# Performance work log

Measured on AMD Instinct MI355X. Metric: run time of the kernel, lower is better.

## Reference

```python
import jax, jax.numpy as jnp
import numpy as np

B, T, D_IN, H = 128, 256, 512, 1024

def setup_inputs() -> dict:
    key = jax.random.key(0)
    ks = jax.random.split(key, 12)
    s = 1.0 / np.sqrt(H)
    return {
        "input": jax.random.normal(ks[0], (B, T, D_IN), jnp.float32),
        "h0": jax.random.normal(ks[1], (B, H), jnp.float32),
        "c0": jax.random.normal(ks[2], (B, H), jnp.float32),
        "ctx": jax.random.normal(ks[3], (B, T, H), jnp.float32),
        "srcmask": jax.random.randint(ks[4], (B, T), 0, 2).astype(bool),
        "W_ih": jax.random.uniform(ks[5], (4 * H, D_IN), jnp.float32, -s, s),
        "W_hh": jax.random.uniform(ks[6], (4 * H, H), jnp.float32, -s, s),
        "b_ih": jax.random.uniform(ks[7], (4 * H,), jnp.float32, -s, s),
        "b_hh": jax.random.uniform(ks[8], (4 * H,), jnp.float32, -s, s),
        "W_attn": jax.random.uniform(ks[9], (H, H), jnp.float32, -s, s),
        "W_out": jax.random.uniform(ks[10], (H, 2 * H), jnp.float32, -s, s),
    }


def reference(input, h0, c0, ctx, srcmask, W_ih, W_hh, b_ih, b_hh, W_attn, W_out):
    def step(carry, x_t):
        h, c = carry
        # LSTMCell: gate order i, f, g, o (PyTorch convention)
        gates = x_t @ W_ih.T + b_ih + h @ W_hh.T + b_hh  # [B, 4H]
        i_g, f_g, g_g, o_g = jnp.split(gates, 4, axis=-1)
        cy = jax.nn.sigmoid(f_g) * c + jax.nn.sigmoid(i_g) * jnp.tanh(g_g)
        hy = jax.nn.sigmoid(o_g) * jnp.tanh(cy)
        # Bilinear attention: score(K_j, q) = K_j^T (W_attn q)
        q = hy @ W_attn.T                                   # [B, H]
        scores = jnp.einsum("blh,bh->bl", ctx, q)          # [B, L]
        scores = jnp.where(srcmask, -jnp.inf, scores)
        probs = jax.nn.softmax(scores, axis=-1)
        wctx = jnp.einsum("bl,blh->bh", probs, ctx)        # [B, H]
        h_tilde = jnp.tanh(jnp.concatenate([wctx, hy], axis=-1) @ W_out.T)
        return (h_tilde, cy), h_tilde

    xs = jnp.transpose(input, (1, 0, 2))  # [T, B, D_IN]
    (h_f, c_f), outs = jax.lax.scan(step, (h0, c0), xs)
    output = jnp.transpose(outs, (1, 0, 2))  # [B, T, H]
    return (output, h_f, c_f)
```

## Files before the change

### kernel.cpp

```cpp
#include <hip/hip_runtime.h>
#include <hip/hip_bf16.h>
#include <math.h>

#define B_  128
#define T_  256
#define DIN 512
#define H_  1024

typedef __attribute__((ext_vector_type(8))) short bf16x8;
typedef __attribute__((ext_vector_type(4))) float f32x4;

#define GLD_LDS16(gsrc, ldst) \
  __builtin_amdgcn_global_load_lds((const __attribute__((address_space(1))) void*)(gsrc), \
                                   (__attribute__((address_space(3))) void*)(ldst), 16, 0, 0)

#define WAITVM_(n) asm volatile("s_waitcnt vmcnt(" #n ")" ::: "memory")
#define WAITVM(n) WAITVM_(n)

__device__ __forceinline__ void split_bf16(float v, __hip_bfloat16* hi, __hip_bfloat16* lo) {
    __hip_bfloat16 h = __float2bfloat16(v);
    *hi = h;
    *lo = __float2bfloat16(v - __bfloat162float(h));
}

__device__ __forceinline__ float sigmoidf_(float x) { return 1.f / (1.f + expf(-x)); }

__global__ void bsum_perm_k(const float* __restrict__ bi, const float* __restrict__ bh,
                            float* __restrict__ o) {
    int c = blockIdx.x * 256 + threadIdx.x;
    int srow = ((c & 3) << 10) | (c >> 2);
    o[c] = bi[srow] + bh[srow];
}

__global__ void detect_mask_k(const int* __restrict__ m, int nwords, int* __restrict__ flag) {
    __shared__ int bad;
    if (threadIdx.x == 0) bad = 0;
    __syncthreads();
    for (int i = threadIdx.x; i < nwords; i += blockDim.x) {
        unsigned v = (unsigned)m[i];
        if (v > 1u) bad = 1;
    }
    __syncthreads();
    if (threadIdx.x == 0) flag[0] = bad ? 0 : 1;
}

__global__ void cvt_split_k(const float* __restrict__ s, __hip_bfloat16* __restrict__ hi,
                            __hip_bfloat16* __restrict__ lo, int n) {
    int i = blockIdx.x * 256 + threadIdx.x;
    if (i < n) split_bf16(s[i], hi + i, lo + i);
}

__global__ void wgp_split_k(const float* __restrict__ Wih, const float* __restrict__ Whh,
                            __hip_bfloat16* __restrict__ Wh, __hip_bfloat16* __restrict__ Wl) {
    long i = (long)blockIdx.x * 256 + threadIdx.x;
    int c = (int)(i / 1536), k = (int)(i - (long)c * 1536);
    int srow = ((c & 3) << 10) | (c >> 2);
    float v = (k < DIN) ? Wih[(long)srow * DIN + k] : Whh[(long)srow * H_ + (k - DIN)];
    split_bf16(v, Wh + i, Wl + i);
}

__global__ void cvtx_k(const float* __restrict__ xsrc, __hip_bfloat16* __restrict__ xh,
                       __hip_bfloat16* __restrict__ xl) {
    int i = blockIdx.x * 256 + threadIdx.x;
    int b = i >> 9, c = i & 511;
    split_bf16(xsrc[(long)b * (T_ * DIN) + c], xh + i, xl + i);
}

constexpr int APL = 128 * 64 * 2;
constexpr int BPL = 32 * 64 * 2;
constexpr int BUFB = 2 * APL + 2 * BPL;
constexpr int LDSZ = 3 * BUFB;

#define GEMM_CORE(NT, NW2, BNV, VMID, NB, KSP, A1H, A1L, LDA1, K1V, A2H, A2L, LDA2, WHP, WLP, LDW) \
    const int n0_ = (NB) * (BNV); \
    const int kbase_ = (KSP) * ((NT) * 64); \
    const int wm_ = (NW2) ? (w >> 1) * 64 : w * 32; \
    const int wn_ = (NW2) ? (w & 1) * 16 : 0; \
    auto stage = [&](int buf, int kt) { \
        char* base = lds + buf * BUFB; \
        const int kb = kbase_ + kt * 64; \
        _Pragma("unroll") \
        for (int pp = 0; pp < 2; ++pp) { \
            const __hip_bfloat16* A1 = pp ? (A1L) : (A1H); \
            const __hip_bfloat16* A2 = pp ? (A2L) : (A2H); \
            _Pragma("unroll") \
            for (int j = 0; j < 4; ++j) { \
                int c = j * 256 + tid; \
                int row = c >> 3, sl2 = c & 7; \
                int e = kb + ((sl2 ^ (row & 7)) << 3); \
                const __hip_bfloat16* src = (e < (K1V)) ? (A1 + (long)row * (LDA1) + e) \
                                                        : (A2 + (long)row * (LDA2) + (e - (K1V))); \
                GLD_LDS16(src, base + pp * APL + ((j * 256 + (tid & 192)) << 4)); \
            } \
            if (tid < (BNV) * 8) { \
                int row = tid >> 3, sl2 = tid & 7; \
                int e = kb + ((sl2 ^ (row & 7)) << 3); \
                const __hip_bfloat16* src = (pp ? (WLP) : (WHP)) + (long)(n0_ + row) * (LDW) + e; \
                GLD_LDS16(src, base + 2 * APL + pp * BPL + ((tid & 192) << 4)); \
            } \
        } \
    }; \
    f32x4 acc[4] = {}; \
    stage(0, 0); \
    if ((NT) > 1) stage(1, 1); \
    for (int kt = 0; kt < (NT); ++kt) { \
        if (kt + 1 < (NT)) { WAITVM(VMID); } else { WAITVM(0); } \
        __builtin_amdgcn_s_barrier(); \
        __builtin_amdgcn_sched_barrier(0); \
        if (kt + 2 < (NT)) stage((kt + 2) % 3, kt + 2); \
        const char* base = lds + (kt % 3) * BUFB; \
        _Pragma("unroll") \
        for (int ks = 0; ks < 2; ++ks) { \
            bf16x8 afh[4], afl[4], bh, bl; \
            _Pragma("unroll") \
            for (int mi = 0; mi < ((NW2) ? 4 : 2); ++mi) { \
                int row = wm_ + mi * 16 + (l & 15); \
                int sl2 = (l >> 4) + ks * 4; \
                int off = row * 128 + ((sl2 ^ (row & 7)) << 4); \
                afh[mi] = *(const bf16x8*)(base + off); \
                afl[mi] = *(const bf16x8*)(base + APL + off); \
            } \
            { \
                int row = wn_ + (l & 15); \
                int sl2 = (l >> 4) + ks * 4; \
                int off = row * 128 + ((sl2 ^ (row & 7)) << 4); \
                bh = *(const bf16x8*)(base + 2 * APL + off); \
                bl = *(const bf16x8*)(base + 2 * APL + BPL + off); \
            } \
            _Pragma("unroll") \
            for (int mi = 0; mi < ((NW2) ? 4 : 2); ++mi) { \
                acc[mi] = __builtin_amdgcn_mfma_f32_16x16x32_bf16(afh[mi], bh, acc[mi], 0, 0, 0); \
                acc[mi] = __builtin_amdgcn_mfma_f32_16x16x32_bf16(afl[mi], bh, acc[mi], 0, 0, 0); \
                acc[mi] = __builtin_amdgcn_mfma_f32_16x16x32_bf16(afh[mi], bl, acc[mi], 0, 0, 0); \
            } \
        } \
    }

__global__ __launch_bounds__(256)
void gemm_g_k(const __hip_bfloat16* __restrict__ xh, const __hip_bfloat16* __restrict__ xl,
              const __hip_bfloat16* __restrict__ hh, const __hip_bfloat16* __restrict__ hl,
              const __hip_bfloat16* __restrict__ Wgh, const __hip_bfloat16* __restrict__ Wgl,
              const float* __restrict__ bsump, float* __restrict__ cbuf,
              __hip_bfloat16* __restrict__ AoBh, __hip_bfloat16* __restrict__ AoBl,
              float* __restrict__ cf,
              const float* __restrict__ input, int t,
              __hip_bfloat16* __restrict__ nxh, __hip_bfloat16* __restrict__ nxl)
{
    __shared__ __attribute__((aligned(16))) char lds[LDSZ];
    const int blk = blockIdx.x, tid = threadIdx.x;
    const int l = tid & 63, w = tid >> 6;

    GEMM_CORE(24, 1, 32, 10, blk, 0,
              xh, xl, DIN, DIN, hh, hl, H_, Wgh, Wgl, (DIN + H_));

    __syncthreads();
    float* sg = (float*)lds;
    {
        float bv = bsump[n0_ + wn_ + (l & 15)];
        #pragma unroll
        for (int mi = 0; mi < 4; ++mi) {
            int rbase = wm_ + mi * 16 + (l >> 4) * 4;
            int col = wn_ + (l & 15);
            #pragma unroll
            for (int r = 0; r < 4; ++r)
                sg[(rbase + r) * 36 + col] = acc[mi][r] + bv;
        }
    }
    __syncthreads();

    #pragma unroll
    for (int k = 0; k < 4; ++k) {
        int ci = k * 256 + tid;
        int b = ci >> 3, jp = ci & 7;
        float4 g4 = *(const float4*)&sg[b * 36 + jp * 4];
        int j = blk * 8 + jp;
        long idx = (long)b * H_ + j;
        float ig = sigmoidf_(g4.x);
        float fg = sigmoidf_(g4.y);
        float gg = tanhf(g4.z);
        float og = sigmoidf_(g4.w);
        float c = fg * cbuf[idx] + ig * gg;
        float h = og * tanhf(c);
        cbuf[idx] = c;
        split_bf16(h, AoBh + (long)b * 2048 + 1024 + j, AoBl + (long)b * 2048 + 1024 + j);
        if (cf) cf[idx] = c;
    }

    if (t + 1 < T_) {
        #pragma unroll
        for (int k = 0; k < 2; ++k) {
            int i2 = blk * 512 + k * 256 + tid;
            int b2 = i2 >> 9, col = i2 & 511;
            float v = input[((long)b2 * T_ + (t + 1)) * DIN + col];
            split_bf16(v, nxh + i2, nxl + i2);
        }
    }
}

__global__ __launch_bounds__(256)
void gemm_q_k(const __hip_bfloat16* __restrict__ AoBh, const __hip_bfloat16* __restrict__ AoBl,
              const __hip_bfloat16* __restrict__ Wah, const __hip_bfloat16* __restrict__ Wal,
              float* __restrict__ qpart)
{
    __shared__ __attribute__((aligned(16))) char lds[LDSZ];
    const int tid = threadIdx.x;
    const int l = tid & 63, w = tid >> 6;

    GEMM_CORE(4, 1, 32, 10, (int)blockIdx.x, (int)blockIdx.y,
              (AoBh + H_), (AoBl + H_), (2 * H_), H_,
              (AoBh + H_), (AoBl + H_), (2 * H_), Wah, Wal, H_);

    float* Cb = qpart + (long)blockIdx.y * (B_ * H_);
    const int n = n0_ + wn_ + (l & 15);
    #pragma unroll
    for (int mi = 0; mi < 4; ++mi) {
        int mbase = wm_ + mi * 16 + (l >> 4) * 4;
        #pragma unroll
        for (int r = 0; r < 4; ++r)
            Cb[(long)(mbase + r) * H_ + n] = acc[mi][r];
    }
}

__global__ __launch_bounds__(256)
void attn_k(const float* __restrict__ ctx, const float* __restrict__ qpart,
            const void* __restrict__ maskp, const int* __restrict__ mflag,
            __hip_bfloat16* __restrict__ AoBh, __hip_bfloat16* __restrict__ AoBl)
{
    constexpr int L = T_, H = H_;
    __shared__ float sacc[4][H_];
    __shared__ float sms[4][2];
    int b = blockIdx.x;
    const float* cb = ctx + (long)b * L * H;
    int tid = threadIdx.x, l = tid & 63, w = tid >> 6;
    int mode = mflag[0];

    float rq[16];
    #pragma unroll
    for (int j = 0; j < 16; ++j) {
        long o = (long)b * H + l + j * 64;
        rq[j] = qpart[o] + qpart[o + 131072] + qpart[o + 262144] + qpart[o + 393216];
    }

    float m = -INFINITY, s = 0.f, acc[16] = {};
    for (int li = w; li < L; li += 4) {
        bool msk = mode ? (((const int*)maskp)[b * L + li] != 0)
                        : (((const unsigned char*)maskp)[b * L + li] != 0);
        if (msk) continue;
        const float* cr = cb + (long)li * H;
        float rc[16], d = 0.f;
        #pragma unroll
        for (int j = 0; j < 16; ++j) { rc[j] = cr[l + j * 64]; d += rc[j] * rq[j]; }
        #pragma unroll
        for (int off = 1; off < 64; off <<= 1) d += __shfl_xor(d, off);
        float mn = fmaxf(m, d);
        float f = expf(m - mn);
        float p = expf(d - mn);
        s = s * f + p;
        #pragma unroll
        for (int j = 0; j < 16; ++j) acc[j] = acc[j] * f + p * rc[j];
        m = mn;
    }

    #pragma unroll
    for (int j = 0; j < 16; ++j) sacc[w][l + j * 64] = acc[j];
    if (l == 0) { sms[w][0] = m; sms[w][1] = s; }
    __syncthreads();

    float M = fmaxf(fmaxf(sms[0][0], sms[1][0]), fmaxf(sms[2][0], sms[3][0]));
    float fw[4], S = 0.f;
    #pragma unroll
    for (int ww = 0; ww < 4; ++ww) {
        fw[ww] = (sms[ww][0] == -INFINITY) ? 0.f : expf(sms[ww][0] - M);
        S += fw[ww] * sms[ww][1];
    }
    float inv = 1.f / S;
    for (int k = tid; k < H; k += 256) {
        float a = sacc[0][k] * fw[0] + sacc[1][k] * fw[1] + sacc[2][k] * fw[2] + sacc[3][k] * fw[3];
        split_bf16(a * inv, AoBh + (long)b * 2048 + k, AoBl + (long)b * 2048 + k);
    }
}

__global__ __launch_bounds__(256)
void gemm_o_k(const __hip_bfloat16* __restrict__ AoBh, const __hip_bfloat16* __restrict__ AoBl,
              const __hip_bfloat16* __restrict__ Woh, const __hip_bfloat16* __restrict__ Wol,
              __hip_bfloat16* __restrict__ hth, __hip_bfloat16* __restrict__ htl,
              float* __restrict__ out, int t, float* __restrict__ hf)
{
    __shared__ __attribute__((aligned(16))) char lds[LDSZ];
    const int tid = threadIdx.x;
    const int l = tid & 63, w = tid >> 6;

    GEMM_CORE(32, 0, 16, 8, (int)blockIdx.x, 0,
              AoBh, AoBl, (2 * H_), (2 * H_),
              AoBh, AoBl, (2 * H_), Woh, Wol, (2 * H_));

    const int j = n0_ + (l & 15);
    #pragma unroll
    for (int mi = 0; mi < 2; ++mi) {
        int bbase = wm_ + mi * 16 + (l >> 4) * 4;
        #pragma unroll
        for (int r = 0; r < 4; ++r) {
            int b = bbase + r;
            float v = tanhf(acc[mi][r]);
            split_bf16(v, hth + (long)b * H_ + j, htl + (long)b * H_ + j);
            out[(long)b * (T_ * H_) + (long)t * H_ + j] = v;
            if (hf) hf[(long)b * H_ + j] = v;
        }
    }
}

extern "C" void kernel_launch(void* const* d_in, const int* in_sizes, int n_in,
                              void* d_out, int out_size, void* d_ws, size_t ws_size,
                              hipStream_t stream)
{
    const float* input  = (const float*)d_in[0];
    const float* h0     = (const float*)d_in[1];
    const float* c0     = (const float*)d_in[2];
    const float* ctx    = (const float*)d_in[3];
    const void*  srcmask= d_in[4];
    const float* W_ih   = (const float*)d_in[5];
    const float* W_hh   = (const float*)d_in[6];
    const float* b_ih   = (const float*)d_in[7];
    const float* b_hh   = (const float*)d_in[8];
    const float* W_attn = (const float*)d_in[9];
    const float* W_out  = (const float*)d_in[10];

    constexpr int B = B_, T = T_, D = DIN, H = H_;

    float* f = (float*)d_ws;
    float* bsump = f; f += 4 * H;
    float* cbuf  = f; f += (size_t)B * H;
    float* qpart = f; f += (size_t)4 * B * H;
    int*   mflag = (int*)f; f += 64;
    __hip_bfloat16* p = (__hip_bfloat16*)f;
    __hip_bfloat16* Wgh = p; p += (size_t)4 * H * (D + H);
    __hip_bfloat16* Wgl = p; p += (size_t)4 * H * (D + H);
    __hip_bfloat16* Wah = p; p += (size_t)H * H;
    __hip_bfloat16* Wal = p; p += (size_t)H * H;
    __hip_bfloat16* Woh = p; p += (size_t)H * 2 * H;
    __hip_bfloat16* Wol = p; p += (size_t)H * 2 * H;
    __hip_bfloat16* hth = p; p += (size_t)B * H;
    __hip_bfloat16* htl = p; p += (size_t)B * H;
    __hip_bfloat16* AoBh = p; p += (size_t)B * 2 * H;
    __hip_bfloat16* AoBl = p; p += (size_t)B * 2 * H;
    __hip_bfloat16* xth[2], *xtl[2];
    xth[0] = p; p += (size_t)B * D;
    xtl[0] = p; p += (size_t)B * D;
    xth[1] = p; p += (size_t)B * D;
    xtl[1] = p; p += (size_t)B * D;

    float* out = (float*)d_out;
    float* hf  = out + (size_t)B * T * H;
    float* cf  = hf + (size_t)B * H;

    hipMemcpyAsync(cbuf, c0, (size_t)B * H * sizeof(float), hipMemcpyDeviceToDevice, stream);
    bsum_perm_k<<<dim3(16), dim3(256), 0, stream>>>(b_ih, b_hh, bsump);
    detect_mask_k<<<dim3(1), dim3(256), 0, stream>>>((const int*)srcmask, B * T / 4, mflag);
    wgp_split_k<<<dim3(4 * H * (D + H) / 256), dim3(256), 0, stream>>>(W_ih, W_hh, Wgh, Wgl);
    cvt_split_k<<<dim3(H * H / 256), dim3(256), 0, stream>>>(W_attn, Wah, Wal, H * H);
    cvt_split_k<<<dim3(H * 2 * H / 256), dim3(256), 0, stream>>>(W_out, Woh, Wol, H * 2 * H);
    cvt_split_k<<<dim3(B * H / 256), dim3(256), 0, stream>>>(h0, hth, htl, B * H);
    cvtx_k<<<dim3(B * D / 256), dim3(256), 0, stream>>>(input, xth[0], xtl[0]);

    dim3 blk(256);
    for (int t = 0; t < T; ++t) {
        int sl = t & 1, sn = sl ^ 1;

        gemm_g_k<<<dim3(128), blk, 0, stream>>>(
            xth[sl], xtl[sl], hth, htl, Wgh, Wgl, bsump, cbuf,
            AoBh, AoBl, (t == T - 1) ? cf : nullptr,
            input, t, xth[sn], xtl[sn]);

        gemm_q_k<<<dim3(32, 4), blk, 0, stream>>>(AoBh, AoBl, Wah, Wal, qpart);

        attn_k<<<dim3(B), blk, 0, stream>>>(ctx, qpart, srcmask, mflag, AoBh, AoBl);

        gemm_o_k<<<dim3(64), blk, 0, stream>>>(
            AoBh, AoBl, Woh, Wol, hth, htl, out, t, (t == T - 1) ? hf : nullptr);
    }
}
```

Before: 21.53 ms.

## Split input projection off the recurrence and overlap independent GEMMs with dependent stages

The fused gate GEMM is split into an x·W_ih part and an h·W_hh part. The x projection for step t+1 is computed inside the attention kernel using the otherwise idle extra blocks. The hy half of the output projection (W_out second half) now runs alongside the attention query GEMM, so the serial post-attention GEMM shrinks to only the attention-context half. This shortens the critical-path work per timestep at the cost of extra fp32 partial-sum buffers and more global traffic.

```diff
diff --git a/kernel.cpp b/kernel.cpp
--- a/kernel.cpp
+++ b/kernel.cpp
@@ -50,20 +50,27 @@
     if (i < n) split_bf16(s[i], hi + i, lo + i);
 }
 
-__global__ void wgp_split_k(const float* __restrict__ Wih, const float* __restrict__ Whh,
-                            __hip_bfloat16* __restrict__ Wh, __hip_bfloat16* __restrict__ Wl) {
+__global__ void wihp_split_k(const float* __restrict__ Wih,
+                             __hip_bfloat16* __restrict__ Wh, __hip_bfloat16* __restrict__ Wl) {
     long i = (long)blockIdx.x * 256 + threadIdx.x;
-    int c = (int)(i / 1536), k = (int)(i - (long)c * 1536);
+    int c = (int)(i >> 9), k = (int)(i & 511);
     int srow = ((c & 3) << 10) | (c >> 2);
-    float v = (k < DIN) ? Wih[(long)srow * DIN + k] : Whh[(long)srow * H_ + (k - DIN)];
-    split_bf16(v, Wh + i, Wl + i);
-}
-
-__global__ void cvtx_k(const float* __restrict__ xsrc, __hip_bfloat16* __restrict__ xh,
-                       __hip_bfloat16* __restrict__ xl) {
+    split_bf16(Wih[(long)srow * DIN + k], Wh + i, Wl + i);
+}
+
+__global__ void whhp_split_k(const float* __restrict__ Whh,
+                             __hip_bfloat16* __restrict__ Wh, __hip_bfloat16* __restrict__ Wl) {
+    long i = (long)blockIdx.x * 256 + threadIdx.x;
+    int c = (int)(i >> 10), k = (int)(i & 1023);
+    int srow = ((c & 3) << 10) | (c >> 2);
+    split_bf16(Whh[(long)srow * H_ + k], Wh + i, Wl + i);
+}
+
+__global__ void cvtx_k(const float* __restrict__ input, int t,
+                       __hip_bfloat16* __restrict__ xh, __hip_bfloat16* __restrict__ xl) {
     int i = blockIdx.x * 256 + threadIdx.x;
     int b = i >> 9, c = i & 511;
-    split_bf16(xsrc[(long)b * (T_ * DIN) + c], xh + i, xl + i);
+    split_bf16(input[((long)b * T_ + t) * DIN + c], xh + i, xl + i);
 }
 
 constexpr int APL = 128 * 64 * 2;
@@ -136,60 +143,86 @@
         } \
     }
 
+__device__ __forceinline__ void xpart_body(char* lds, int ct, int tid, int l, int w,
+                                           const __hip_bfloat16* xh, const __hip_bfloat16* xl,
+                                           const __hip_bfloat16* Wih_h, const __hip_bfloat16* Wih_l,
+                                           float* xp)
+{
+    GEMM_CORE(8, 1, 32, 10, ct, 0, xh, xl, DIN, DIN, xh, xl, DIN, Wih_h, Wih_l, DIN);
+    const int n = n0_ + wn_ + (l & 15);
+    #pragma unroll
+    for (int mi = 0; mi < 4; ++mi) {
+        int rb = wm_ + mi * 16 + (l >> 4) * 4;
+        #pragma unroll
+        for (int r = 0; r < 4; ++r)
+            xp[(long)(rb + r) * 4096 + n] = acc[mi][r];
+    }
+}
+
 __global__ __launch_bounds__(256)
-void gemm_g_k(const __hip_bfloat16* __restrict__ xh, const __hip_bfloat16* __restrict__ xl,
-              const __hip_bfloat16* __restrict__ hh, const __hip_bfloat16* __restrict__ hl,
-              const __hip_bfloat16* __restrict__ Wgh, const __hip_bfloat16* __restrict__ Wgl,
-              const float* __restrict__ bsump, float* __restrict__ cbuf,
-              __hip_bfloat16* __restrict__ AoBh, __hip_bfloat16* __restrict__ AoBl,
-              float* __restrict__ cf,
-              const float* __restrict__ input, int t,
-              __hip_bfloat16* __restrict__ nxh, __hip_bfloat16* __restrict__ nxl)
+void xpart_k(const __hip_bfloat16* __restrict__ xh, const __hip_bfloat16* __restrict__ xl,
+             const __hip_bfloat16* __restrict__ Wih_h, const __hip_bfloat16* __restrict__ Wih_l,
+             float* __restrict__ xp)
+{
+    __shared__ __attribute__((aligned(16))) char lds[LDSZ];
+    const int tid = threadIdx.x, l = tid & 63, w = tid >> 6;
+    xpart_body(lds, blockIdx.x, tid, l, w, xh, xl, Wih_h, Wih_l, xp);
+}
+
+__global__ __launch_bounds__(256)
+void n1_k(const __hip_bfloat16* __restrict__ hh, const __hip_bfloat16* __restrict__ hl,
+          const __hip_bfloat16* __restrict__ Whh_h, const __hip_bfloat16* __restrict__ Whh_l,
+          const float* __restrict__ bsump, const float* __restrict__ xpart,
+          float* __restrict__ cbuf,
+          __hip_bfloat16* __restrict__ AoBh, __hip_bfloat16* __restrict__ AoBl,
+          float* __restrict__ cf,
+          const float* __restrict__ input, int t,
+          __hip_bfloat16* __restrict__ nxh, __hip_bfloat16* __restrict__ nxl)
 {
     __shared__ __attribute__((aligned(16))) char lds[LDSZ];
     const int blk = blockIdx.x, tid = threadIdx.x;
     const int l = tid & 63, w = tid >> 6;
 
-    GEMM_CORE(24, 1, 32, 10, blk, 0,
-              xh, xl, DIN, DIN, hh, hl, H_, Wgh, Wgl, (DIN + H_));
-
-    __syncthreads();
-    float* sg = (float*)lds;
-    {
-        float bv = bsump[n0_ + wn_ + (l & 15)];
-        #pragma unroll
-        for (int mi = 0; mi < 4; ++mi) {
-            int rbase = wm_ + mi * 16 + (l >> 4) * 4;
-            int col = wn_ + (l & 15);
-            #pragma unroll
-            for (int r = 0; r < 4; ++r)
-                sg[(rbase + r) * 36 + col] = acc[mi][r] + bv;
-        }
-    }
-    __syncthreads();
-
-    #pragma unroll
-    for (int k = 0; k < 4; ++k) {
-        int ci = k * 256 + tid;
-        int b = ci >> 3, jp = ci & 7;
-        float4 g4 = *(const float4*)&sg[b * 36 + jp * 4];
-        int j = blk * 8 + jp;
-        long idx = (long)b * H_ + j;
-        float ig = sigmoidf_(g4.x);
-        float fg = sigmoidf_(g4.y);
-        float gg = tanhf(g4.z);
-        float og = sigmoidf_(g4.w);
-        float c = fg * cbuf[idx] + ig * gg;
-        float h = og * tanhf(c);
-        cbuf[idx] = c;
-        split_bf16(h, AoBh + (long)b * 2048 + 1024 + j, AoBl + (long)b * 2048 + 1024 + j);
-        if (cf) cf[idx] = c;
-    }
-
-    if (t + 1 < T_) {
+    if (blk < 128) {
+        GEMM_CORE(16, 1, 32, 10, blk, 0, hh, hl, H_, H_, hh, hl, H_, Whh_h, Whh_l, H_);
+
+        __syncthreads();
+        float* sg = (float*)lds;
+        {
+            int colg = n0_ + wn_ + (l & 15);
+            int coll = wn_ + (l & 15);
+            float bv = bsump[colg];
+            #pragma unroll
+            for (int mi = 0; mi < 4; ++mi) {
+                int rb = wm_ + mi * 16 + (l >> 4) * 4;
+                #pragma unroll
+                for (int r = 0; r < 4; ++r)
+                    sg[(rb + r) * 36 + coll] = acc[mi][r] + xpart[(long)(rb + r) * 4096 + colg] + bv;
+            }
+        }
+        __syncthreads();
+
+        #pragma unroll
+        for (int k = 0; k < 4; ++k) {
+            int ci = k * 256 + tid;
+            int b = ci >> 3, jp = ci & 7;
+            float4 g4 = *(const float4*)&sg[b * 36 + jp * 4];
+            int j = blk * 8 + jp;
+            long idx = (long)b * H_ + j;
+            float ig = sigmoidf_(g4.x);
+            float fg = sigmoidf_(g4.y);
+            float gg = tanhf(g4.z);
+            float og = sigmoidf_(g4.w);
+            float c = fg * cbuf[idx] + ig * gg;
+            float h = og * tanhf(c);
+            cbuf[idx] = c;
+            split_bf16(h, AoBh + (long)b * 2048 + 1024 + j, AoBl + (long)b * 2048 + 1024 + j);
+            if (cf) cf[idx] = c;
+        }
+    } else if (t + 1 < T_) {
         #pragma unroll
         for (int k = 0; k < 2; ++k) {
-            int i2 = blk * 512 + k * 256 + tid;
+            int i2 = (blk - 128) * 512 + k * 256 + tid;
             int b2 = i2 >> 9, col = i2 & 511;
             float v = input[((long)b2 * T_ + (t + 1)) * DIN + col];
             split_bf16(v, nxh + i2, nxl + i2);
@@ -198,99 +231,128 @@
 }
 
 __global__ __launch_bounds__(256)
-void gemm_q_k(const __hip_bfloat16* __restrict__ AoBh, const __hip_bfloat16* __restrict__ AoBl,
-              const __hip_bfloat16* __restrict__ Wah, const __hip_bfloat16* __restrict__ Wal,
-              float* __restrict__ qpart)
+void n2_k(const __hip_bfloat16* __restrict__ AoBh, const __hip_bfloat16* __restrict__ AoBl,
+          const __hip_bfloat16* __restrict__ Wah, const __hip_bfloat16* __restrict__ Wal,
+          const __hip_bfloat16* __restrict__ Woh, const __hip_bfloat16* __restrict__ Wol,
+          float* __restrict__ qpart, float* __restrict__ opart)
+{
+    __shared__ __attribute__((aligned(16))) char lds[LDSZ];
+    const int blk = blockIdx.x, tid = threadIdx.x;
+    const int l = tid & 63, w = tid >> 6;
+
+    if (blk < 128) {
+        const int ct = blk & 31, ksp = blk >> 5;
+        GEMM_CORE(4, 1, 32, 10, ct, ksp,
+                  (AoBh + H_), (AoBl + H_), (2 * H_), (2 * H_),
+                  (AoBh + H_), (AoBl + H_), (2 * H_), Wah, Wal, H_);
+        float* Cb = qpart + (long)ksp * (B_ * H_);
+        const int n = n0_ + wn_ + (l & 15);
+        #pragma unroll
+        for (int mi = 0; mi < 4; ++mi) {
+            int rb = wm_ + mi * 16 + (l >> 4) * 4;
+            #pragma unroll
+            for (int r = 0; r < 4; ++r)
+                Cb[(long)(rb + r) * H_ + n] = acc[mi][r];
+        }
+    } else {
+        const int ct = (blk - 128) & 31, ksp = (blk - 128) >> 5;
+        GEMM_CORE(4, 1, 32, 10, ct, ksp,
+                  (AoBh + H_), (AoBl + H_), (2 * H_), (4 * H_),
+                  (AoBh + H_), (AoBl + H_), (2 * H_),
+                  (Woh + H_), (Wol + H_), (2 * H_));
+        float* Cb = opart + (long)ksp * (B_ * H_);
+        const int n = n0_ + wn_ + (l & 15);
+        #pragma unroll
+        for (int mi = 0; mi < 4; ++mi) {
+            int rb = wm_ + mi * 16 + (l >> 4) * 4;
+            #pragma unroll
+            for (int r = 0; r < 4; ++r)
+                Cb[(long)(rb + r) * H_ + n] = acc[mi][r];
+        }
+    }
+}
+
+__global__ __launch_bounds__(256)
+void n3_k(const float* __restrict__ ctx, const float* __restrict__ qpart,
+          const void* __restrict__ maskp, const int* __restrict__ mflag,
+          __hip_bfloat16* __restrict__ AoBh, __hip_bfloat16* __restrict__ AoBl,
+          const __hip_bfloat16* __restrict__ nxh, const __hip_bfloat16* __restrict__ nxl,
+          const __hip_bfloat16* __restrict__ Wih_h, const __hip_bfloat16* __restrict__ Wih_l,
+          float* __restrict__ xpnext, int last)
+{
+    __shared__ __attribute__((aligned(16))) char lds[LDSZ];
+    const int blk = blockIdx.x, tid = threadIdx.x;
+    const int l = tid & 63, w = tid >> 6;
+
+    if (blk < 128) {
+        const int b = blk;
+        const float* cb = ctx + (long)b * (T_ * H_);
+        const int mode = mflag[0];
+
+        float rq[16];
+        #pragma unroll
+        for (int j = 0; j < 16; ++j) {
+            long o = (long)b * H_ + l + j * 64;
+            rq[j] = qpart[o] + qpart[o + 131072] + qpart[o + 262144] + qpart[o + 393216];
+        }
+
+        float m = -INFINITY, s = 0.f, acc[16] = {};
+        for (int li = w; li < T_; li += 4) {
+            bool msk = mode ? (((const int*)maskp)[b * T_ + li] != 0)
+                            : (((const unsigned char*)maskp)[b * T_ + li] != 0);
+            if (msk) continue;
+            const float* cr = cb + (long)li * H_;
+            float rc[16], d = 0.f;
+            #pragma unroll
+            for (int j = 0; j < 16; ++j) { rc[j] = cr[l + j * 64]; d += rc[j] * rq[j]; }
+            #pragma unroll
+            for (int off = 1; off < 64; off <<= 1) d += __shfl_xor(d, off);
+            float mn = fmaxf(m, d);
+            float f = expf(m - mn);
+            float p = expf(d - mn);
+            s = s * f + p;
+            #pragma unroll
+            for (int j = 0; j < 16; ++j) acc[j] = acc[j] * f + p * rc[j];
+            m = mn;
+        }
+
+        float (*sacc)[H_] = (float (*)[H_])lds;
+        float (*sms)[2] = (float (*)[2])(lds + 4 * H_ * sizeof(float));
+        #pragma unroll
+        for (int j = 0; j < 16; ++j) sacc[w][l + j * 64] = acc[j];
+        if (l == 0) { sms[w][0] = m; sms[w][1] = s; }
+        __syncthreads();
+
+        float M = fmaxf(fmaxf(sms[0][0], sms[1][0]), fmaxf(sms[2][0], sms[3][0]));
+        float fw[4], S = 0.f;
+        #pragma unroll
+        for (int ww = 0; ww < 4; ++ww) {
+            fw[ww] = (sms[ww][0] == -INFINITY) ? 0.f : expf(sms[ww][0] - M);
+            S += fw[ww] * sms[ww][1];
+        }
+        float inv = 1.f / S;
+        for (int k = tid; k < H_; k += 256) {
+            float a = (sacc[0][k] * fw[0] + sacc[1][k] * fw[1] +
+                       sacc[2][k] * fw[2] + sacc[3][k] * fw[3]) * inv;
+            split_bf16(a, AoBh + (long)b * 2048 + k, AoBl + (long)b * 2048 + k);
+        }
+    } else if (!last) {
+        xpart_body(lds, blk - 128, tid, l, w, nxh, nxl, Wih_h, Wih_l, xpnext);
+    }
+}
+
+__global__ __launch_bounds__(256)
+void n4_k(const __hip_bfloat16* __restrict__ AoBh, const __hip_bfloat16* __restrict__ AoBl,
+          const __hip_bfloat16* __restrict__ Woh, const __hip_bfloat16* __restrict__ Wol,
+          const float* __restrict__ opart,
+          __hip_bfloat16* __restrict__ hth, __hip_bfloat16* __restrict__ htl,
+          float* __restrict__ out, int t, float* __restrict__ hf)
 {
     __shared__ __attribute__((aligned(16))) char lds[LDSZ];
     const int tid = threadIdx.x;
     const int l = tid & 63, w = tid >> 6;
 
-    GEMM_CORE(4, 1, 32, 10, (int)blockIdx.x, (int)blockIdx.y,
-              (AoBh + H_), (AoBl + H_), (2 * H_), H_,
-              (AoBh + H_), (AoBl + H_), (2 * H_), Wah, Wal, H_);
-
-    float* Cb = qpart + (long)blockIdx.y * (B_ * H_);
-    const int n = n0_ + wn_ + (l & 15);
-    #pragma unroll
-    for (int mi = 0; mi < 4; ++mi) {
-        int mbase = wm_ + mi * 16 + (l >> 4) * 4;
-        #pragma unroll
-        for (int r = 0; r < 4; ++r)
-            Cb[(long)(mbase + r) * H_ + n] = acc[mi][r];
-    }
-}
-
-__global__ __launch_bounds__(256)
-void attn_k(const float* __restrict__ ctx, const float* __restrict__ qpart,
-            const void* __restrict__ maskp, const int* __restrict__ mflag,
-            __hip_bfloat16* __restrict__ AoBh, __hip_bfloat16* __restrict__ AoBl)
-{
-    constexpr int L = T_, H = H_;
-    __shared__ float sacc[4][H_];
-    __shared__ float sms[4][2];
-    int b = blockIdx.x;
-    const float* cb = ctx + (long)b * L * H;
-    int tid = threadIdx.x, l = tid & 63, w = tid >> 6;
-    int mode = mflag[0];
-
-    float rq[16];
-    #pragma unroll
-    for (int j = 0; j < 16; ++j) {
-        long o = (long)b * H + l + j * 64;
-        rq[j] = qpart[o] + qpart[o + 131072] + qpart[o + 262144] + qpart[o + 393216];
-    }
-
-    float m = -INFINITY, s = 0.f, acc[16] = {};
-    for (int li = w; li < L; li += 4) {
-        bool msk = mode ? (((const int*)maskp)[b * L + li] != 0)
-                        : (((const unsigned char*)maskp)[b * L + li] != 0);
-        if (msk) continue;
-        const float* cr = cb + (long)li * H;
-        float rc[16], d = 0.f;
-        #pragma unroll
-        for (int j = 0; j < 16; ++j) { rc[j] = cr[l + j * 64]; d += rc[j] * rq[j]; }
-        #pragma unroll
-        for (int off = 1; off < 64; off <<= 1) d += __shfl_xor(d, off);
-        float mn = fmaxf(m, d);
-        float f = expf(m - mn);
-        float p = expf(d - mn);
-        s = s * f + p;
-        #pragma unroll
-        for (int j = 0; j < 16; ++j) acc[j] = acc[j] * f + p * rc[j];
-        m = mn;
-    }
-
-    #pragma unroll
-    for (int j = 0; j < 16; ++j) sacc[w][l + j * 64] = acc[j];
-    if (l == 0) { sms[w][0] = m; sms[w][1] = s; }
-    __syncthreads();
-
-    float M = fmaxf(fmaxf(sms[0][0], sms[1][0]), fmaxf(sms[2][0], sms[3][0]));
-    float fw[4], S = 0.f;
-    #pragma unroll
-    for (int ww = 0; ww < 4; ++ww) {
-        fw[ww] = (sms[ww][0] == -INFINITY) ? 0.f : expf(sms[ww][0] - M);
-        S += fw[ww] * sms[ww][1];
-    }
-    float inv = 1.f / S;
-    for (int k = tid; k < H; k += 256) {
-        float a = sacc[0][k] * fw[0] + sacc[1][k] * fw[1] + sacc[2][k] * fw[2] + sacc[3][k] * fw[3];
-        split_bf16(a * inv, AoBh + (long)b * 2048 + k, AoBl + (long)b * 2048 + k);
-    }
-}
-
-__global__ __launch_bounds__(256)
-void gemm_o_k(const __hip_bfloat16* __restrict__ AoBh, const __hip_bfloat16* __restrict__ AoBl,
-              const __hip_bfloat16* __restrict__ Woh, const __hip_bfloat16* __restrict__ Wol,
-              __hip_bfloat16* __restrict__ hth, __hip_bfloat16* __restrict__ htl,
-              float* __restrict__ out, int t, float* __restrict__ hf)
-{
-    __shared__ __attribute__((aligned(16))) char lds[LDSZ];
-    const int tid = threadIdx.x;
-    const int l = tid & 63, w = tid >> 6;
-
-    GEMM_CORE(32, 0, 16, 8, (int)blockIdx.x, 0,
+    GEMM_CORE(16, 0, 16, 8, (int)blockIdx.x, 0,
               AoBh, AoBl, (2 * H_), (2 * H_),
               AoBh, AoBl, (2 * H_), Woh, Wol, (2 * H_));
 
@@ -301,10 +363,13 @@
         #pragma unroll
         for (int r = 0; r < 4; ++r) {
             int b = bbase + r;
-            float v = tanhf(acc[mi][r]);
-            split_bf16(v, hth + (long)b * H_ + j, htl + (long)b * H_ + j);
+            long o = (long)b * H_ + j;
+            float v = acc[mi][r] + opart[o] + opart[o + 131072]
+                                + opart[o + 262144] + opart[o + 393216];
+            v = tanhf(v);
+            split_bf16(v, hth + o, htl + o);
             out[(long)b * (T_ * H_) + (long)t * H_ + j] = v;
-            if (hf) hf[(long)b * H_ + j] = v;
+            if (hf) hf[o] = v;
         }
     }
 }
@@ -331,10 +396,15 @@
     float* bsump = f; f += 4 * H;
     float* cbuf  = f; f += (size_t)B * H;
     float* qpart = f; f += (size_t)4 * B * H;
+    float* opart = f; f += (size_t)4 * B * H;
+    float* xpart0 = f; f += (size_t)B * 4 * H;
+    float* xpart1 = f; f += (size_t)B * 4 * H;
     int*   mflag = (int*)f; f += 64;
     __hip_bfloat16* p = (__hip_bfloat16*)f;
-    __hip_bfloat16* Wgh = p; p += (size_t)4 * H * (D + H);
-    __hip_bfloat16* Wgl = p; p += (size_t)4 * H * (D + H);
+    __hip_bfloat16* Wihh = p; p += (size_t)4 * H * D;
+    __hip_bfloat16* Wihl = p; p += (size_t)4 * H * D;
+    __hip_bfloat16* Whhh = p; p += (size_t)4 * H * H;
+    __hip_bfloat16* Whhl = p; p += (size_t)4 * H * H;
     __hip_bfloat16* Wah = p; p += (size_t)H * H;
     __hip_bfloat16* Wal = p; p += (size_t)H * H;
     __hip_bfloat16* Woh = p; p += (size_t)H * 2 * H;
@@ -343,11 +413,11 @@
     __hip_bfloat16* htl = p; p += (size_t)B * H;
     __hip_bfloat16* AoBh = p; p += (size_t)B * 2 * H;
     __hip_bfloat16* AoBl = p; p += (size_t)B * 2 * H;
-    __hip_bfloat16* xth[2], *xtl[2];
-    xth[0] = p; p += (size_t)B * D;
-    xtl[0] = p; p += (size_t)B * D;
-    xth[1] = p; p += (size_t)B * D;
-    xtl[1] = p; p += (size_t)B * D;
+    __hip_bfloat16* xph[2], *xpl[2];
+    xph[0] = p; p += (size_t)B * D;
+    xpl[0] = p; p += (size_t)B * D;
+    xph[1] = p; p += (size_t)B * D;
+    xpl[1] = p; p += (size_t)B * D;
 
     float* out = (float*)d_out;
     float* hf  = out + (size_t)B * T * H;
@@ -356,26 +426,33 @@
     hipMemcpyAsync(cbuf, c0, (size_t)B * H * sizeof(float), hipMemcpyDeviceToDevice, stream);
     bsum_perm_k<<<dim3(16), dim3(256), 0, stream>>>(b_ih, b_hh, bsump);
     detect_mask_k<<<dim3(1), dim3(256), 0, stream>>>((const int*)srcmask, B * T / 4, mflag);
-    wgp_split_k<<<dim3(4 * H * (D + H) / 256), dim3(256), 0, stream>>>(W_ih, W_hh, Wgh, Wgl);
+    wihp_split_k<<<dim3(4 * H * D / 256), dim3(256), 0, stream>>>(W_ih, Wihh, Wihl);
+    whhp_split_k<<<dim3(4 * H * H / 256), dim3(256), 0, stream>>>(W_hh, Whhh, Whhl);
     cvt_split_k<<<dim3(H * H / 256), dim3(256), 0, stream>>>(W_attn, Wah, Wal, H * H);
     cvt_split_k<<<dim3(H * 2 * H / 256), dim3(256), 0, stream>>>(W_out, Woh, Wol, H * 2 * H);
     cvt_split_k<<<dim3(B * H / 256), dim3(256), 0, stream>>>(h0, hth, htl, B * H);
-    cvtx_k<<<dim3(B * D / 256), dim3(256), 0, stream>>>(input, xth[0], xtl[0]);
+    cvtx_k<<<dim3(B * D / 256), dim3(256), 0, stream>>>(input, 0, xph[0], xpl[0]);
+    xpart_k<<<dim3(128), dim3(256), 0, stream>>>(xph[0], xpl[0], Wihh, Wihl, xpart0);
 
     dim3 blk(256);
     for (int t = 0; t < T; ++t) {
-        int sl = t & 1, sn = sl ^ 1;
-
-        gemm_g_k<<<dim3(128), blk, 0, stream>>>(
-            xth[sl], xtl[sl], hth, htl, Wgh, Wgl, bsump, cbuf,
+        float* xp_cur  = (t & 1) ? xpart1 : xpart0;
+        float* xp_next = (t & 1) ? xpart0 : xpart1;
+        int sn = (t + 1) & 1;
+
+        n1_k<<<dim3(256), blk, 0, stream>>>(
+            hth, htl, Whhh, Whhl, bsump, xp_cur, cbuf,
             AoBh, AoBl, (t == T - 1) ? cf : nullptr,
-            input, t, xth[sn], xtl[sn]);
-
-        gemm_q_k<<<dim3(32, 4), blk, 0, stream>>>(AoBh, AoBl, Wah, Wal, qpart);
-
-        attn_k<<<dim3(B), blk, 0, stream>>>(ctx, qpart, srcmask, mflag, AoBh, AoBl);
-
-        gemm_o_k<<<dim3(64), blk, 0, stream>>>(
-            AoBh, AoBl, Woh, Wol, hth, htl, out, t, (t == T - 1) ? hf : nullptr);
-    }
-}
+            input, t, xph[sn], xpl[sn]);
+
+        n2_k<<<dim3(256), blk, 0, stream>>>(AoBh, AoBl, Wah, Wal, Woh, Wol, qpart, opart);
+
+        n3_k<<<dim3(256), blk, 0, stream>>>(
+            ctx, qpart, srcmask, mflag, AoBh, AoBl,
+            xph[sn], xpl[sn], Wihh, Wihl, xp_next, (t == T - 1) ? 1 : 0);
+
+        n4_k<<<dim3(64), blk, 0, stream>>>(
+            AoBh, AoBl, Woh, Wol, opart, hth, htl,
+            out, t, (t == T - 1) ? hf : nullptr);
+    }
+}
```

Result: faster. 19.36 ms (-10.1%).
